# Optimization experiments

Hardware: AMD Instinct MI355X
Metric: run time of the kernel (lower is better)

## Reference

```python
import jax, jax.numpy as jnp
import numpy as np

B, S, D, H, DFF = 4, 2048, 2048, 16, 8192
DH = D // H
THETA = 10000.0
EPS = 1e-5


def rmsnorm(x, g):
    return x * jax.lax.rsqrt(jnp.mean(x * x, axis=-1, keepdims=True) + EPS) * g


def rope(x, pos):
    # x: [B, H, S, DH]; rotate interleaved even/odd pairs
    half = DH // 2
    inv_freq = THETA ** (-(jnp.arange(half, dtype=jnp.float32) * 2.0) / DH)  # [half]
    ang = pos.astype(jnp.float32)[:, None] * inv_freq  # [S, half]
    cos, sin = jnp.cos(ang), jnp.sin(ang)
    x1, x2 = x[..., 0::2], x[..., 1::2]
    r1 = x1 * cos - x2 * sin
    r2 = x1 * sin + x2 * cos
    return jnp.stack([r1, r2], axis=-1).reshape(x.shape)


def setup_inputs() -> dict:
    key = jax.random.key(0)
    ks = jax.random.split(key, 12)
    s = 0.02
    return {
        "x": jax.random.normal(ks[0], (B, S, D), dtype=jnp.float32),
        "attention_mask": jnp.ones((S, S), dtype=bool),
        "wq": jax.random.normal(ks[1], (D, D), dtype=jnp.float32) * s,
        "wk": jax.random.normal(ks[2], (D, D), dtype=jnp.float32) * s,
        "wv": jax.random.normal(ks[3], (D, D), dtype=jnp.float32) * s,
        "wo": jax.random.normal(ks[4], (D, D), dtype=jnp.float32) * s,
        "w1": jax.random.normal(ks[5], (DFF, D), dtype=jnp.float32) * s,
        "w2": jax.random.normal(ks[6], (D, DFF), dtype=jnp.float32) * s,
        "w3": jax.random.normal(ks[7], (DFF, D), dtype=jnp.float32) * s,
        "g1": jnp.ones((D,), dtype=jnp.float32),
        "g2": jnp.ones((D,), dtype=jnp.float32),
    }


def reference(x, attention_mask, wq, wk, wv, wo, w1, w2, w3, g1, g2):
    pos = jnp.arange(x.shape[-2])
    # pre-norm attention
    h = rmsnorm(x, g1)
    q = (h @ wq.T).reshape(B, S, H, DH).transpose(0, 2, 1, 3)
    k = (h @ wk.T).reshape(B, S, H, DH).transpose(0, 2, 1, 3)
    v = (h @ wv.T).reshape(B, S, H, DH).transpose(0, 2, 1, 3)
    q = rope(q, pos)
    k = rope(k, pos)
    scores = jnp.einsum("bhqd,bhkd->bhqk", q, k) / np.float32(np.sqrt(DH))
    scores = jnp.where(attention_mask, scores, jnp.float32(-1e9))
    attn = jax.nn.softmax(scores, axis=-1)
    o = jnp.einsum("bhqk,bhkd->bhqd", attn, v)
    o = o.transpose(0, 2, 1, 3).reshape(B, S, D) @ wo.T
    x = x + o
    # pre-norm SwiGLU FFN
    h2 = rmsnorm(x, g2)
    ffn = (jax.nn.silu(h2 @ w1.T) * (h2 @ w3.T)) @ w2.T
    return x + ffn
```

## Files before the change

### kernel.cpp

```cpp
#include <hip/hip_runtime.h>
#include <cstdint>
#include <cstddef>

#define B_   4
#define S_   2048
#define D_   2048
#define H_   16
#define DH_  128
#define DFF_ 8192
#define LOG2E 1.4426950408889634f

typedef __bf16 bf16_t;
typedef __bf16 bf16x4 __attribute__((ext_vector_type(4)));
typedef __bf16 bf16x8 __attribute__((ext_vector_type(8)));
typedef float  f32x4  __attribute__((ext_vector_type(4)));

#define MFMA16 __builtin_amdgcn_mfma_f32_16x16x32_bf16

__device__ __forceinline__ void glds16(const void* g, void* l) {
  __builtin_amdgcn_global_load_lds((__attribute__((address_space(1))) void*)g,
                                   (__attribute__((address_space(3))) void*)l,
                                   16, 0, 0);
}

__global__ __launch_bounds__(256) void cvt_kernel(const float* __restrict__ in,
                                                  bf16_t* __restrict__ out, int n8) {
  int i = blockIdx.x * 256 + threadIdx.x;
  if (i >= n8) return;
  const float4* p4 = (const float4*)in;
  float4 a = p4[2 * (size_t)i];
  float4 b = p4[2 * (size_t)i + 1];
  bf16x8 o;
  o[0] = (bf16_t)a.x; o[1] = (bf16_t)a.y; o[2] = (bf16_t)a.z; o[3] = (bf16_t)a.w;
  o[4] = (bf16_t)b.x; o[5] = (bf16_t)b.y; o[6] = (bf16_t)b.z; o[7] = (bf16_t)b.w;
  ((bf16x8*)out)[i] = o;
}

__global__ __launch_bounds__(256) void rmsnorm_kernel(const float* __restrict__ x,
                                                      const float* __restrict__ g,
                                                      bf16_t* __restrict__ out) {
  const int row = blockIdx.x, tid = threadIdx.x;
  const float* xr = x + (size_t)row * D_;
  float4 a = ((const float4*)xr)[tid * 2];
  float4 b = ((const float4*)xr)[tid * 2 + 1];
  float ss = a.x*a.x + a.y*a.y + a.z*a.z + a.w*a.w
           + b.x*b.x + b.y*b.y + b.z*b.z + b.w*b.w;
#pragma unroll
  for (int m = 1; m < 64; m <<= 1) ss += __shfl_xor(ss, m);
  __shared__ float red[4];
  if ((tid & 63) == 0) red[tid >> 6] = ss;
  __syncthreads();
  float tot = red[0] + red[1] + red[2] + red[3];
  float rms = rsqrtf(tot * (1.0f / D_) + 1e-5f);
  float4 ga = ((const float4*)g)[tid * 2];
  float4 gb = ((const float4*)g)[tid * 2 + 1];
  bf16x8 o;
  o[0] = (bf16_t)(a.x * rms * ga.x); o[1] = (bf16_t)(a.y * rms * ga.y);
  o[2] = (bf16_t)(a.z * rms * ga.z); o[3] = (bf16_t)(a.w * rms * ga.w);
  o[4] = (bf16_t)(b.x * rms * gb.x); o[5] = (bf16_t)(b.y * rms * gb.y);
  o[6] = (bf16_t)(b.z * rms * gb.z); o[7] = (bf16_t)(b.w * rms * gb.w);
  ((bf16x8*)out)[(size_t)row * 256 + tid] = o;
}

template <int EPI>
__global__ __launch_bounds__(512, 4) void gemm256h(const bf16_t* __restrict__ A,
                                                   const bf16_t* __restrict__ W,
                                                   const float* __restrict__ addf,
                                                   const bf16_t* __restrict__ addb,
                                                   bf16_t* __restrict__ outb,
                                                   bf16_t* __restrict__ outb2,
                                                   bf16_t* __restrict__ outb3,
                                                   float* __restrict__ outf,
                                                   int M, int N, int K) {
  __shared__ char ldsb[49152];
  const int tid = threadIdx.x;
  const int wid = tid >> 6, l = tid & 63, l15 = l & 15, lg = l >> 4;
  const int wm = wid >> 2, wn = wid & 3;

  const int nwg = gridDim.x;
  int wg = (int)blockIdx.x;
  wg = (wg & 7) * (nwg >> 3) + (wg >> 3);
  const int ntm = M >> 7;
  const int wide = 4 * ntm;
  const int grp = wg / wide;
  const int rem = wg % wide;
  const int m0 = (rem >> 2) << 7;
  const int n0 = ((grp << 2) + (rem & 3)) << 8;

  f32x4 acc[4][4];
  const f32x4 z4 = {0.f, 0.f, 0.f, 0.f};
#pragma unroll
  for (int i = 0; i < 4; i++)
#pragma unroll
    for (int j = 0; j < 4; j++) acc[i][j] = z4;

  const int o0 = tid * 16;
  const int srow = o0 >> 7;
  const int ssw = ((o0 & 127) ^ ((srow & 7) << 4)) >> 1;
  const bf16_t* Asrc = A + (size_t)(m0 + srow) * K + ssw;
  const bf16_t* Wsrc = W + (size_t)(n0 + srow) * K + ssw;
  const int rsw = (l15 & 7) << 4;
  const int acol0 = (lg * 16) ^ rsw;
  const int acol1 = (64 + lg * 16) ^ rsw;

  const int NT = K >> 6;
  for (int t = 0; t < NT; t++) {
    const bf16_t* as = Asrc + (size_t)t * 64;
    glds16(as, ldsb + o0);
    glds16(as + 64 * (size_t)K, ldsb + 8192 + o0);
    const bf16_t* ws = Wsrc + (size_t)t * 64;
    glds16(ws, ldsb + 16384 + o0);
    glds16(ws + 64 * (size_t)K, ldsb + 24576 + o0);
    glds16(ws + 128 * (size_t)K, ldsb + 32768 + o0);
    glds16(ws + 192 * (size_t)K, ldsb + 40960 + o0);
    asm volatile("s_waitcnt vmcnt(0)" ::: "memory");
    __builtin_amdgcn_s_barrier();
    __builtin_amdgcn_sched_barrier(0);
    bf16x8 af[4][2];
#pragma unroll
    for (int fi = 0; fi < 4; fi++) {
      const char* p = ldsb + (wm * 64 + fi * 16 + l15) * 128;
      af[fi][0] = *(const bf16x8*)(p + acol0);
      af[fi][1] = *(const bf16x8*)(p + acol1);
    }
    __builtin_amdgcn_s_setprio(1);
#pragma unroll
    for (int n = 0; n < 4; n++) {
      const char* p = ldsb + 16384 + (wn * 64 + n * 16 + l15) * 128;
      bf16x8 b0 = *(const bf16x8*)(p + acol0);
      bf16x8 b1 = *(const bf16x8*)(p + acol1);
#pragma unroll
      for (int m = 0; m < 4; m++) {
        acc[m][n] = MFMA16(af[m][0], b0, acc[m][n], 0, 0, 0);
        acc[m][n] = MFMA16(af[m][1], b1, acc[m][n], 0, 0, 0);
      }
    }
    __builtin_amdgcn_s_setprio(0);
    __builtin_amdgcn_sched_barrier(0);
    __builtin_amdgcn_s_barrier();
  }

#pragma unroll
  for (int m = 0; m < 4; m++) {
    const int gr = m0 + wm * 64 + m * 16 + lg * 4;
#pragma unroll
    for (int n = 0; n < 4; n++) {
      const int gc = n0 + wn * 64 + n * 16 + l15;
      if constexpr (EPI == 4) {
        const int seg = gc >> 11;
        const int gcl = gc & 2047;
        if (seg < 2) {
          bf16_t* o = seg ? outb2 : outb;
#pragma unroll
          for (int r = 0; r < 4; r++)
            o[(size_t)(gr + r) * D_ + gcl] = (bf16_t)acc[m][n][r];
        } else {
          const int bb = gr >> 11, ss = gr & 2047;
          bf16x4 pk;
#pragma unroll
          for (int r = 0; r < 4; r++) pk[r] = (bf16_t)acc[m][n][r];
          *(bf16x4*)(outb3 + ((size_t)bb * D_ + gcl) * S_ + ss) = pk;
        }
      } else {
#pragma unroll
        for (int r = 0; r < 4; r++) {
          size_t idx = (size_t)(gr + r) * N + gc;
          if constexpr (EPI == 0) {
            outb[idx] = (bf16_t)acc[m][n][r];
          } else if constexpr (EPI == 1) {
            outf[idx] = acc[m][n][r] + addf[idx];
          } else {
            float a1v = (float)addb[idx];
            outb[idx] = (bf16_t)(a1v / (1.0f + expf(-a1v)) * acc[m][n][r]);
          }
        }
      }
    }
  }
}

__global__ __launch_bounds__(256) void rope_kernel(bf16_t* __restrict__ buf) {
  size_t i = (size_t)blockIdx.x * 256 + threadIdx.x;
  int pi = (int)(i & 63);
  size_t rh = i >> 6;
  int srow = (int)((rh / H_) % S_);
  float inv = expf((float)pi * (-9.210340371976184f / 64.0f));
  float ang = (float)srow * inv;
  float c = cosf(ang), sn = sinf(ang);
  bf16_t* p = buf + i * 2;
  float x1 = (float)p[0], x2 = (float)p[1];
  p[0] = (bf16_t)(x1 * c - x2 * sn);
  p[1] = (bf16_t)(x1 * sn + x2 * c);
}

__global__ __launch_bounds__(256) void attn_kernel(const bf16_t* __restrict__ Q,
                                                   const bf16_t* __restrict__ Kb,
                                                   const bf16_t* __restrict__ Vt,
                                                   bf16_t* __restrict__ O) {
  const int qt = blockIdx.x, h = blockIdx.y, b = blockIdx.z;
  const int tid = threadIdx.x;
  const int wid = tid >> 6, l = tid & 63, l15 = l & 15, lg = l >> 4;

  __shared__ bf16_t Klds[64 * 128];
  __shared__ bf16_t Vlds[128 * 64];
  __shared__ bf16_t Plds[4][16 * 72];

  const int q0 = qt * 64 + wid * 16;
  const f32x4 z4 = {0.f, 0.f, 0.f, 0.f};
  const float SCL = 0.08838834764831845f * LOG2E;

  bf16x8 qf[4];
  {
    const bf16_t* qp = Q + ((size_t)(b * S_ + q0 + l15)) * D_ + h * DH_ + lg * 8;
#pragma unroll
    for (int kk = 0; kk < 4; kk++) qf[kk] = *(const bf16x8*)(qp + kk * 32);
  }
  f32x4 of[8];
#pragma unroll
  for (int f = 0; f < 8; f++) of[f] = z4;
  float m_run = -1e30f, l_run = 0.f;

  const int o0 = tid * 16;
  const int krow0 = o0 >> 8;
  const int scol = ((o0 & 255) ^ ((krow0 & 7) << 4)) >> 1;
  const int vrow0 = o0 >> 7;
  const int vcol = ((o0 & 127) ^ ((vrow0 & 7) << 4)) >> 1;

  const size_t bh_off = ((size_t)b * S_) * D_ + (size_t)h * DH_;
  const bf16_t* vtbase = Vt + ((size_t)b * D_ + h * DH_) * S_;

  for (int kv0 = 0; kv0 < S_; kv0 += 64) {
    const bf16_t* kbase = Kb + bh_off + (size_t)kv0 * D_;
#pragma unroll
    for (int s = 0; s < 4; s++)
      glds16(kbase + (size_t)(krow0 + 16 * s) * D_ + scol,
             (char*)Klds + s * 4096 + wid * 1024);
#pragma unroll
    for (int s = 0; s < 4; s++)
      glds16(vtbase + (size_t)(vrow0 + 32 * s) * S_ + kv0 + vcol,
             (char*)Vlds + s * 4096 + wid * 1024);
    __syncthreads();

    f32x4 st[4];
#pragma unroll
    for (int c = 0; c < 4; c++) {
      st[c] = z4;
      const int row = c * 16 + l15;
      const char* kr = (const char*)Klds + row * 256;
      const int sw = (row & 7) << 4;
#pragma unroll
      for (int kk = 0; kk < 4; kk++) {
        bf16x8 kf = *(const bf16x8*)(kr + ((kk * 64 + lg * 16) ^ sw));
        st[c] = MFMA16(kf, qf[kk], st[c], 0, 0, 0);
      }
    }

    float s[16];
#pragma unroll
    for (int c = 0; c < 4; c++)
#pragma unroll
      for (int r = 0; r < 4; r++) s[c * 4 + r] = st[c][r] * SCL;
    float pm = s[0];
#pragma unroll
    for (int i = 1; i < 16; i++) pm = fmaxf(pm, s[i]);
    pm = fmaxf(pm, __shfl_xor(pm, 16));
    pm = fmaxf(pm, __shfl_xor(pm, 32));
    if (!__all(pm - m_run <= 8.0f)) {
      float mnew = fmaxf(m_run, pm);
      float alpha = exp2f(m_run - mnew);
      float aq[4];
#pragma unroll
      for (int r = 0; r < 4; r++) aq[r] = __shfl(alpha, lg * 4 + r);
#pragma unroll
      for (int f = 0; f < 8; f++)
#pragma unroll
        for (int r = 0; r < 4; r++) of[f][r] *= aq[r];
      l_run *= alpha;
      m_run = mnew;
    }
    float p[16], ts = 0.f;
#pragma unroll
    for (int i = 0; i < 16; i++) { p[i] = exp2f(s[i] - m_run); ts += p[i]; }
    ts += __shfl_xor(ts, 16);
    ts += __shfl_xor(ts, 32);
    l_run += ts;

    bf16_t* pw = &Plds[wid][0];
#pragma unroll
    for (int c = 0; c < 4; c++)
#pragma unroll
      for (int r = 0; r < 4; r++)
        pw[l15 * 72 + c * 16 + lg * 4 + r] = (bf16_t)p[c * 4 + r];
    asm volatile("s_waitcnt lgkmcnt(0)" ::: "memory");
    bf16x8 pa0 = *(const bf16x8*)(pw + l15 * 72 + lg * 8);
    bf16x8 pa1 = *(const bf16x8*)(pw + l15 * 72 + 32 + lg * 8);
#pragma unroll
    for (int f = 0; f < 8; f++) {
      const int row = 16 * f + l15;
      const char* vr = (const char*)Vlds + row * 128;
      const int sw = (row & 7) << 4;
      bf16x8 bv0 = *(const bf16x8*)(vr + ((lg * 16) ^ sw));
      bf16x8 bv1 = *(const bf16x8*)(vr + ((64 + lg * 16) ^ sw));
      of[f] = MFMA16(pa0, bv0, of[f], 0, 0, 0);
      of[f] = MFMA16(pa1, bv1, of[f], 0, 0, 0);
    }
    __syncthreads();
  }

  float inv[4];
#pragma unroll
  for (int r = 0; r < 4; r++) inv[r] = 1.0f / __shfl(l_run, lg * 4 + r);
#pragma unroll
  for (int f = 0; f < 8; f++)
#pragma unroll
    for (int r = 0; r < 4; r++)
      O[((size_t)(b * S_ + q0 + lg * 4 + r)) * D_ + h * DH_ + 16 * f + l15] =
          (bf16_t)(of[f][r] * inv[r]);
}

extern "C" void kernel_launch(void* const* d_in, const int* in_sizes, int n_in,
                              void* d_out, int out_size, void* d_ws, size_t ws_size,
                              hipStream_t stream) {
  const float* x  = (const float*)d_in[0];
  const float* wq = (const float*)d_in[2];
  const float* wk = (const float*)d_in[3];
  const float* wv = (const float*)d_in[4];
  const float* wo = (const float*)d_in[5];
  const float* w1 = (const float*)d_in[6];
  const float* w2 = (const float*)d_in[7];
  const float* w3 = (const float*)d_in[8];
  const float* g1 = (const float*)d_in[9];
  const float* g2 = (const float*)d_in[10];
  float* out = (float*)d_out;

  const size_t ND = (size_t)D_ * D_;
  const size_t NF = (size_t)DFF_ * D_;
  const size_t SLOT = NF * 2;
  char* base = (char*)d_ws;
  bf16_t* wslot = (bf16_t*)(base);
  bf16_t* h1    = (bf16_t*)(base + 1 * SLOT);
  bf16_t* qb    = (bf16_t*)(base + 2 * SLOT);
  bf16_t* kb    = (bf16_t*)(base + 3 * SLOT);
  bf16_t* vt    = (bf16_t*)(base + 4 * SLOT);
  bf16_t* ob    = (bf16_t*)(base + 5 * SLOT);
  bf16_t* h2    = h1;
  bf16_t* g     = qb;
  float*  x1    = out;

  auto cvt = [&](const float* in, bf16_t* o, size_t n) {
    int n8 = (int)(n / 8);
    cvt_kernel<<<(n8 + 255) / 256, 256, 0, stream>>>(in, o, n8);
  };

  rmsnorm_kernel<<<B_ * S_, 256, 0, stream>>>(x, g1, h1);

  cvt(wq, wslot, ND);
  cvt(wk, wslot + ND, ND);
  cvt(wv, wslot + 2 * ND, ND);
  const int gqkv3 = (8192 / 128) * (6144 / 256);
  gemm256h<4><<<gqkv3, 512, 0, stream>>>(h1, wslot, nullptr, nullptr,
                                         qb, kb, vt, nullptr, 8192, 6144, 2048);

  rope_kernel<<<(B_ * S_ * H_ * 64) / 256, 256, 0, stream>>>(qb);
  rope_kernel<<<(B_ * S_ * H_ * 64) / 256, 256, 0, stream>>>(kb);

  dim3 ga(S_ / 64, H_, B_);
  attn_kernel<<<ga, 256, 0, stream>>>(qb, kb, vt, ob);

  const int gd = (8192 / 128) * (2048 / 256);
  cvt(wo, wslot, ND);
  gemm256h<1><<<gd, 512, 0, stream>>>(ob, wslot, x, nullptr,
                                      nullptr, nullptr, nullptr, x1, 8192, 2048, 2048);

  rmsnorm_kernel<<<B_ * S_, 256, 0, stream>>>(x1, g2, h2);

  const int gffh = (8192 / 128) * (8192 / 256);
  cvt(w1, wslot, NF);
  gemm256h<0><<<gffh, 512, 0, stream>>>(h2, wslot, nullptr, nullptr,
                                        g, nullptr, nullptr, nullptr, 8192, 8192, 2048);

  cvt(w3, wslot, NF);
  gemm256h<2><<<gffh, 512, 0, stream>>>(h2, wslot, nullptr, g,
                                        g, nullptr, nullptr, nullptr, 8192, 8192, 2048);

  cvt(w2, wslot, NF);
  gemm256h<1><<<gd, 512, 0, stream>>>(g, wslot, x1, nullptr,
                                      nullptr, nullptr, nullptr, x1, 8192, 2048, 8192);
}
```

Before: 1.405 ms.

## Add double-buffered GEMM variant with XCD remap for FFN up projections

Adds a specialized 128x256-tile GEMM kernel with BK=32, a two-stage LDS double buffer filled by direct global-to-LDS loads, a swizzled LDS layout, and a workgroup index remap that spreads tiles across XCDs and groups them for L2 reuse. Launch bounds request 4 blocks per CU to raise occupancy. It is used for the w1 and w3 FFN GEMMs in place of the generic kernel. The goal is to overlap memory loads with MFMA work and cut pipeline stalls, at the cost of a short K-step and possible register pressure from the occupancy target.

Result: slower. 1.457 ms (+3.7%).

```diff
diff --git a/kernel.cpp b/kernel.cpp
--- a/kernel.cpp
+++ b/kernel.cpp
@@ -179,6 +179,101 @@
   }
 }
 
+template <int EPI>
+__global__ __launch_bounds__(512, 4) void gemm256h2(const bf16_t* __restrict__ A,
+                                                    const bf16_t* __restrict__ W,
+                                                    const bf16_t* __restrict__ addb,
+                                                    bf16_t* __restrict__ outb,
+                                                    int M, int N, int K) {
+  __shared__ char ldsb[49152];
+  const int tid = threadIdx.x;
+  const int wid = tid >> 6, l = tid & 63, l15 = l & 15, lg = l >> 4;
+  const int wm = wid >> 2, wn = wid & 3;
+
+  const int nwg = gridDim.x;
+  int wg = (int)blockIdx.x;
+  wg = (wg & 7) * (nwg >> 3) + (wg >> 3);
+  const int ntm = M >> 7;
+  const int wide = 4 * ntm;
+  const int grp = wg / wide;
+  const int rem = wg % wide;
+  const int m0 = (rem >> 2) << 7;
+  const int n0 = ((grp << 2) + (rem & 3)) << 8;
+
+  f32x4 acc[4][4];
+  const f32x4 z4 = {0.f, 0.f, 0.f, 0.f};
+#pragma unroll
+  for (int i = 0; i < 4; i++)
+#pragma unroll
+    for (int j = 0; j < 4; j++) acc[i][j] = z4;
+
+  const int o0 = tid * 16;
+  const int srow = o0 >> 6;
+  const int ssw = ((o0 & 63) ^ ((srow & 3) << 4)) >> 1;
+  const bf16_t* Asrc = A + (size_t)(m0 + srow) * K + ssw;
+  const bf16_t* Wsrc = W + (size_t)(n0 + srow) * K + ssw;
+  const int rsw = (l15 & 3) << 4;
+  const int acol = (lg * 16) ^ rsw;
+
+#define H2_STAGE(d, kt)                                                       \
+  do {                                                                        \
+    const bf16_t* a_ = Asrc + (size_t)(kt) * 32;                              \
+    glds16(a_, ldsb + (d) * 24576 + o0);                                      \
+    const bf16_t* w_ = Wsrc + (size_t)(kt) * 32;                              \
+    glds16(w_, ldsb + (d) * 24576 + 8192 + o0);                               \
+    glds16(w_ + 128 * (size_t)K, ldsb + (d) * 24576 + 16384 + o0);            \
+  } while (0)
+
+  const int NT = K >> 5;
+  H2_STAGE(0, 0);
+  H2_STAGE(1, 1);
+
+  for (int t = 0; t < NT; t++) {
+    const int d = t & 1;
+    if (t + 1 < NT) asm volatile("s_waitcnt vmcnt(3)" ::: "memory");
+    else            asm volatile("s_waitcnt vmcnt(0)" ::: "memory");
+    __builtin_amdgcn_s_barrier();
+    __builtin_amdgcn_sched_barrier(0);
+    const char* ab = ldsb + d * 24576;
+    bf16x8 af[4];
+#pragma unroll
+    for (int m = 0; m < 4; m++)
+      af[m] = *(const bf16x8*)(ab + (wm * 64 + m * 16 + l15) * 64 + acol);
+    __builtin_amdgcn_s_setprio(1);
+#pragma unroll
+    for (int n = 0; n < 4; n++) {
+      bf16x8 bf = *(const bf16x8*)(ab + 8192 + (wn * 64 + n * 16 + l15) * 64 + acol);
+#pragma unroll
+      for (int m = 0; m < 4; m++)
+        acc[m][n] = MFMA16(af[m], bf, acc[m][n], 0, 0, 0);
+    }
+    __builtin_amdgcn_s_setprio(0);
+    __builtin_amdgcn_sched_barrier(0);
+    __builtin_amdgcn_s_barrier();
+    if (t + 2 < NT) H2_STAGE(d, t + 2);
+  }
+
+#pragma unroll
+  for (int m = 0; m < 4; m++) {
+    const int gr = m0 + wm * 64 + m * 16 + lg * 4;
+#pragma unroll
+    for (int n = 0; n < 4; n++) {
+      const int gc = n0 + wn * 64 + n * 16 + l15;
+#pragma unroll
+      for (int r = 0; r < 4; r++) {
+        size_t idx = (size_t)(gr + r) * N + gc;
+        if constexpr (EPI == 0) {
+          outb[idx] = (bf16_t)acc[m][n][r];
+        } else {
+          float a1v = (float)addb[idx];
+          outb[idx] = (bf16_t)(a1v / (1.0f + expf(-a1v)) * acc[m][n][r]);
+        }
+      }
+    }
+  }
+#undef H2_STAGE
+}
+
 __global__ __launch_bounds__(256) void rope_kernel(bf16_t* __restrict__ buf) {
   size_t i = (size_t)blockIdx.x * 256 + threadIdx.x;
   int pi = (int)(i & 63);
@@ -376,12 +471,10 @@
 
   const int gffh = (8192 / 128) * (8192 / 256);
   cvt(w1, wslot, NF);
-  gemm256h<0><<<gffh, 512, 0, stream>>>(h2, wslot, nullptr, nullptr,
-                                        g, nullptr, nullptr, nullptr, 8192, 8192, 2048);
+  gemm256h2<0><<<gffh, 512, 0, stream>>>(h2, wslot, nullptr, g, 8192, 8192, 2048);
 
   cvt(w3, wslot, NF);
-  gemm256h<2><<<gffh, 512, 0, stream>>>(h2, wslot, nullptr, g,
-                                        g, nullptr, nullptr, nullptr, 8192, 8192, 2048);
+  gemm256h2<2><<<gffh, 512, 0, stream>>>(h2, wslot, g, g, 8192, 8192, 2048);
 
   cvt(w2, wslot, NF);
   gemm256h<1><<<gd, 512, 0, stream>>>(g, wslot, x1, nullptr,
```
